# Performance work log

Hardware: AMD Instinct MI355X
Metric: run time of the kernel (lower is better)

Reference implementation:

```python
import jax, jax.numpy as jnp
import numpy as np

S, B, D, N, DH = 2048, 2, 1024, 16, 64  # seq, batch, d_model, n_head, d_head
LN_EPS = 1e-5


def setup_inputs() -> dict:
    key = jax.random.key(0)
    ks = jax.random.split(key, 8)
    h = jax.random.normal(ks[0], (S, B, D), dtype=jnp.float32)
    Wq = jax.random.normal(ks[1], (D, N * DH), dtype=jnp.float32) * 0.02
    Wkv = jax.random.normal(ks[2], (D, 2 * N * DH), dtype=jnp.float32) * 0.02
    Wo = jax.random.normal(ks[3], (N * DH, D), dtype=jnp.float32) * 0.02
    ln_gamma = jnp.ones((D,), dtype=jnp.float32)
    ln_beta = jnp.zeros((D,), dtype=jnp.float32)
    # persistent compressive-memory state from a previous segment
    memory = jax.random.normal(ks[4], (B, N, DH, DH), dtype=jnp.float32)
    # normalization is a sum of (elu(k)+1) over ~S positions -> strictly positive, O(S)
    mem_norm = jax.random.uniform(ks[5], (B, 1, N, DH), dtype=jnp.float32) * S + 1.0
    gate_beta = jnp.ones((1,), dtype=jnp.float32) * 0.01  # beta_eps
    return {"h": h, "Wq": Wq, "Wkv": Wkv, "Wo": Wo, "ln_gamma": ln_gamma,
            "ln_beta": ln_beta, "memory": memory, "mem_norm": mem_norm,
            "gate_beta": gate_beta}


def reference(h, Wq, Wkv, Wo, ln_gamma, ln_beta, memory, mem_norm, gate_beta):
    scale = 1.0 / np.sqrt(DH).astype(np.float32)
    # projections (pre_lnorm=False, mems=None -> c == h)
    q = (h @ Wq).reshape(S, B, N, DH)
    k, v = jnp.split(h @ Wkv, 2, axis=-1)
    k = k.reshape(S, B, N, DH)
    v = v.reshape(S, B, N, DH)
    # local quadratic attention
    score = jnp.einsum('ibnd,jbnd->ijbn', q, k) * scale  # [S,S,B,N]
    prob = jax.nn.softmax(score, axis=1)
    attn_vec = jnp.einsum('ijbn,jbnd->ibnd', prob, v).reshape(S, B, N * DH)
    # memory retrieval (NOTE: source swaps K/V in the _update_memory call;
    # it is done under no_grad -> stop_gradient here)
    cached_Q = jax.nn.elu(q.swapaxes(0, 1)) + 1.0          # [B,S,N,DH]
    num = jnp.einsum('bsnk,bnkv->bsnv', cached_Q, memory)   # [B,S,N,DH]
    den = jnp.einsum('bsnk,bvnk->bsnv', cached_Q, mem_norm)  # [B,S,N,1]
    content_A = jax.lax.stop_gradient(num / den)            # [B,S,N,DH]
    # gated injection
    g = jax.nn.sigmoid(gate_beta)                           # [1]
    inj = g * content_A.swapaxes(0, 1).reshape(S, B, N * DH) + (1.0 - g) * attn_vec
    attn_out = inj @ Wo
    # post layernorm residual
    y = h + attn_out
    mu = jnp.mean(y, axis=-1, keepdims=True)
    var = jnp.mean((y - mu) ** 2, axis=-1, keepdims=True)
    return (y - mu) / jnp.sqrt(var + LN_EPS) * ln_gamma + ln_beta
```

## Files before the change

kernel.cpp:

```cpp
#include <hip/hip_runtime.h>


typedef unsigned short ushort_t;
typedef unsigned int uint32;

typedef __bf16 bf16x8 __attribute__((ext_vector_type(8)));
typedef float f32x4 __attribute__((ext_vector_type(4)));
typedef float f32x16 __attribute__((ext_vector_type(16)));
typedef unsigned short u16x8 __attribute__((ext_vector_type(8)));
typedef unsigned short u16x4 __attribute__((ext_vector_type(4)));
typedef unsigned int u32x4 __attribute__((ext_vector_type(4)));

typedef const __attribute__((address_space(1))) void gvoid_t;
typedef __attribute__((address_space(3))) void lvoid_t;

#define S_LEN 2048
#define BATCH 2
#define NHEAD 16

__device__ __forceinline__ ushort_t f2bf(float x) {
  union { float f; unsigned u; } c; c.f = x;
  unsigned r = (c.u + 0x7FFFu + ((c.u >> 16) & 1u)) >> 16;
  return (ushort_t)r;
}
__device__ __forceinline__ float bf2f(ushort_t v) {
  union { unsigned u; float f; } c; c.u = ((unsigned)v) << 16;
  return c.f;
}

__global__ __launch_bounds__(256) void k_cvt_h(const float* __restrict__ src,
                                               ushort_t* __restrict__ dst, int n4) {
  int idx = blockIdx.x * 256 + threadIdx.x;
  if (idx >= n4) return;
  float4 v = ((const float4*)src)[idx];
  u16x4 o; o[0] = f2bf(v.x); o[1] = f2bf(v.y); o[2] = f2bf(v.z); o[3] = f2bf(v.w);
  ((u16x4*)dst)[idx] = o;
}

__global__ __launch_bounds__(256) void k_cvt_wT3(const float* __restrict__ Wq,
                                                 const float* __restrict__ Wkv,
                                                 const float* __restrict__ Wo,
                                                 ushort_t* __restrict__ wT,
                                                 ushort_t* __restrict__ woT) {
  const int z = blockIdx.z;
  const float* W;
  ushort_t* WT;
  int N;
  if (z == 0)      { W = Wq;  WT = wT;                          N = 1024; }
  else if (z == 1) { W = Wkv; WT = wT + (size_t)1024 * 1024;    N = 2048; }
  else             { W = Wo;  WT = woT;                         N = 1024; }
  const int K = 1024;
  if (blockIdx.x * 32 >= N) return;
  __shared__ float tile[32][33];
  const int n0 = blockIdx.x * 32, k0 = blockIdx.y * 32;
  const int tx = threadIdx.x & 31, ty = threadIdx.x >> 5;
#pragma unroll
  for (int r = 0; r < 32; r += 8)
    tile[ty + r][tx] = W[(size_t)(k0 + ty + r) * N + n0 + tx];
  __syncthreads();
#pragma unroll
  for (int r = 0; r < 32; r += 8)
    WT[(size_t)(n0 + ty + r) * K + k0 + tx] = f2bf(tile[tx][ty + r]);
}

template <int OUT_BF16>
__global__ __launch_bounds__(256) void k_gemm_bt(const ushort_t* __restrict__ A,
                                                 const ushort_t* __restrict__ B,
                                                 void* __restrict__ Cv, int M, int N, int K,
                                                 int nbx) {
  __shared__ __attribute__((aligned(16))) ushort_t As[128 * 32];
  __shared__ __attribute__((aligned(16))) ushort_t Bs[128 * 32];
  const int per = gridDim.x >> 3;
  const int fl = (blockIdx.x & 7) * per + (blockIdx.x >> 3);
  const int m0 = (fl / nbx) * 128, n0 = (fl % nbx) * 128;
  const int tid = threadIdx.x, w = tid >> 6, lane = tid & 63;
  const int wm = (w >> 1) * 64, wn = (w & 1) * 64;
  const int l15 = lane & 15, l4 = lane >> 4;
  f32x4 acc[4][4];
#pragma unroll
  for (int i = 0; i < 4; ++i)
#pragma unroll
    for (int j = 0; j < 4; ++j)
#pragma unroll
      for (int r = 0; r < 4; ++r) acc[i][j][r] = 0.f;

  for (int k0 = 0; k0 < K; k0 += 32) {
    __syncthreads();
#pragma unroll
    for (int r = 0; r < 2; ++r) {
      int c = r * 256 + w * 64 + lane;
      const ushort_t* ga = A + (size_t)(m0 + (c >> 2)) * K + k0 + (c & 3) * 8;
      const ushort_t* gb = B + (size_t)(n0 + (c >> 2)) * K + k0 + (c & 3) * 8;
      __builtin_amdgcn_global_load_lds((gvoid_t*)ga, (lvoid_t*)(As + (r * 256 + w * 64) * 8), 16, 0, 0);
      __builtin_amdgcn_global_load_lds((gvoid_t*)gb, (lvoid_t*)(Bs + (r * 256 + w * 64) * 8), 16, 0, 0);
    }
    __syncthreads();
    bf16x8 af[4], bfr[4];
#pragma unroll
    for (int i = 0; i < 4; ++i) af[i] = *(const bf16x8*)&As[(wm + i * 16 + l15) * 32 + l4 * 8];
#pragma unroll
    for (int j = 0; j < 4; ++j) bfr[j] = *(const bf16x8*)&Bs[(wn + j * 16 + l15) * 32 + l4 * 8];
#pragma unroll
    for (int i = 0; i < 4; ++i)
#pragma unroll
      for (int j = 0; j < 4; ++j)
        acc[i][j] = __builtin_amdgcn_mfma_f32_16x16x32_bf16(af[i], bfr[j], acc[i][j], 0, 0, 0);
  }
#pragma unroll
  for (int i = 0; i < 4; ++i)
#pragma unroll
    for (int j = 0; j < 4; ++j)
#pragma unroll
      for (int r = 0; r < 4; ++r) {
        int row = m0 + wm + i * 16 + l4 * 4 + r;
        int col = n0 + wn + j * 16 + l15;
        if (OUT_BF16)
          ((ushort_t*)Cv)[(size_t)row * N + col] = f2bf(acc[i][j][r]);
        else
          ((float*)Cv)[(size_t)row * N + col] = acc[i][j][r];
      }
}

__global__ __launch_bounds__(256) void k_gemm64(const ushort_t* __restrict__ A,
                                                const ushort_t* __restrict__ B,
                                                float* __restrict__ C, int M, int N, int K,
                                                int nbx) {
  __shared__ __attribute__((aligned(16))) ushort_t As[64 * 32];
  __shared__ __attribute__((aligned(16))) ushort_t Bs[128 * 32];
  const int per = gridDim.x >> 3;
  const int fl = (blockIdx.x & 7) * per + (blockIdx.x >> 3);
  const int m0 = (fl / nbx) * 64, n0 = (fl % nbx) * 128;
  const int tid = threadIdx.x, w = tid >> 6, lane = tid & 63;
  const int wn = w * 32;
  const int l15 = lane & 15, l4 = lane >> 4;
  f32x4 acc[4][2];
#pragma unroll
  for (int i = 0; i < 4; ++i)
#pragma unroll
    for (int j = 0; j < 2; ++j)
#pragma unroll
      for (int r = 0; r < 4; ++r) acc[i][j][r] = 0.f;

  for (int k0 = 0; k0 < K; k0 += 32) {
    __syncthreads();
    {
      int c = w * 64 + lane;
      const ushort_t* ga = A + (size_t)(m0 + (c >> 2)) * K + k0 + (c & 3) * 8;
      __builtin_amdgcn_global_load_lds((gvoid_t*)ga, (lvoid_t*)(As + w * 512), 16, 0, 0);
#pragma unroll
      for (int r = 0; r < 2; ++r) {
        int c2 = r * 256 + w * 64 + lane;
        const ushort_t* gb = B + (size_t)(n0 + (c2 >> 2)) * K + k0 + (c2 & 3) * 8;
        __builtin_amdgcn_global_load_lds((gvoid_t*)gb, (lvoid_t*)(Bs + r * 2048 + w * 512), 16, 0, 0);
      }
    }
    __syncthreads();
    bf16x8 af[4], bfr[2];
#pragma unroll
    for (int i = 0; i < 4; ++i) af[i] = *(const bf16x8*)&As[(i * 16 + l15) * 32 + l4 * 8];
#pragma unroll
    for (int j = 0; j < 2; ++j) bfr[j] = *(const bf16x8*)&Bs[(wn + j * 16 + l15) * 32 + l4 * 8];
#pragma unroll
    for (int i = 0; i < 4; ++i)
#pragma unroll
      for (int j = 0; j < 2; ++j)
        acc[i][j] = __builtin_amdgcn_mfma_f32_16x16x32_bf16(af[i], bfr[j], acc[i][j], 0, 0, 0);
  }
#pragma unroll
  for (int i = 0; i < 4; ++i)
#pragma unroll
    for (int j = 0; j < 2; ++j)
#pragma unroll
      for (int r = 0; r < 4; ++r)
        C[(size_t)(m0 + i * 16 + l4 * 4 + r) * N + n0 + wn + j * 16 + l15] = acc[i][j][r];
}

__global__ __launch_bounds__(256) void k_vt(const ushort_t* __restrict__ qkv,
                                            ushort_t* __restrict__ vt) {
  __shared__ uint32 tile[64 * 65];
  const int jt = blockIdx.x, bn = blockIdx.y, b = bn & 1, n = bn >> 1;
  const int tid = threadIdx.x;
  const int j0 = jt * 64;
#pragma unroll
  for (int rr = 0; rr < 2; ++rr) {
    int lin = rr * 2048 + tid * 8;
    int j = lin >> 6, d0 = lin & 63;
    u16x8 v = *(const u16x8*)(qkv + (size_t)(j0 + j) * 6144 + b * 3072 + 2048 + n * 64 + d0);
#pragma unroll
    for (int e = 0; e < 8; ++e) tile[j * 65 + d0 + e] = v[e];
  }
  __syncthreads();
#pragma unroll
  for (int rr = 0; rr < 2; ++rr) {
    int lin = rr * 2048 + tid * 8;
    int d = lin >> 6, jj = lin & 63;
    u16x8 o;
#pragma unroll
    for (int e = 0; e < 8; ++e) o[e] = (ushort_t)tile[(jj + e) * 65 + d];
    *(u16x8*)(vt + ((size_t)bn * 64 + d) * 2048 + j0 + jj) = o;
  }
}

__device__ __forceinline__ void stage_k(const ushort_t* __restrict__ qkv, ushort_t* kw,
                                        int j0, int b, int n, int w, int lane) {
#pragma unroll
  for (int r = 0; r < 2; ++r) {
    int jb_ = w * 16 + r * 8;
    int jb8 = w * 2 + r;
    const ushort_t* ksrc = qkv + (size_t)(j0 + jb_ + (lane >> 3)) * 6144 + b * 3072 + n * 64 + 1024
                           + ((((lane & 7) ^ (lane >> 3) ^ jb8) & 7) << 3);
    __builtin_amdgcn_global_load_lds((gvoid_t*)ksrc, (lvoid_t*)(kw + jb_ * 64), 16, 0, 0);
  }
}
__device__ __forceinline__ void stage_vt(const ushort_t* __restrict__ vt, ushort_t* vw,
                                         int j0, int bn, int w, int lane) {
#pragma unroll
  for (int r = 0; r < 2; ++r) {
    int db_ = w * 16 + r * 8;
    int jb8 = w * 2 + r;
    const ushort_t* vsrc = vt + ((size_t)bn * 64 + db_ + (lane >> 3)) * 2048 + j0
                           + ((((lane & 7) ^ (lane >> 3) ^ jb8) & 7) << 3);
    __builtin_amdgcn_global_load_lds((gvoid_t*)vsrc, (lvoid_t*)(vw + db_ * 64), 16, 0, 0);
  }
}

__global__ __launch_bounds__(256, 4) void k_attn(const ushort_t* __restrict__ qkv,
                                                 const ushort_t* __restrict__ vt,
                                                 ushort_t* o0, ushort_t* o1,
                                                 float* __restrict__ l0,
                                                 float* __restrict__ l1) {
  __shared__ __attribute__((aligned(16))) ushort_t Ks[2][4096];
  __shared__ __attribute__((aligned(16))) ushort_t VTs[2][4096];
  const int bn = blockIdx.y, b = bn & 1, n = bn >> 1, z = blockIdx.z;
  const int tid = threadIdx.x, w = tid >> 6, lane = tid & 63;
  const int l31 = lane & 31, h = lane >> 5;
  const int qrow = blockIdx.x * 128 + w * 32 + l31;
  const size_t qoff = (size_t)qrow * 6144 + b * 3072 + n * 64;
  const float CEXP = 0.18033688011113723f;
  bf16x8 qf[4];
#pragma unroll
  for (int ks = 0; ks < 4; ++ks) {
    u16x8 qv = *(const u16x8*)(qkv + qoff + ks * 16 + h * 8);
    union { u16x8 u; bf16x8 v; } cu;
#pragma unroll
    for (int e = 0; e < 8; ++e) cu.u[e] = f2bf(bf2f(qv[e]) * CEXP);
    qf[ks] = cu.v;
  }
  const int fA = (l31 & 7) ^ (l31 >> 3);
  const int fB = fA ^ 4;

  const int t0 = z * 16;
  stage_k(qkv, Ks[0], t0 * 64, b, n, w, lane);
  stage_vt(vt, VTs[0], t0 * 64, bn, w, lane);
  __syncthreads();

  f32x16 oacc[2];
#pragma unroll
  for (int r = 0; r < 16; ++r) { oacc[0][r] = 0.f; oacc[1][r] = 0.f; }
  float lsum = 0.f;

  for (int t = 0; t < 16; ++t) {
    const ushort_t* Kb = Ks[t & 1];
    const ushort_t* Vb = VTs[t & 1];
    if (t < 15) {
      stage_k(qkv, Ks[(t + 1) & 1], (t0 + t + 1) * 64, b, n, w, lane);
      stage_vt(vt, VTs[(t + 1) & 1], (t0 + t + 1) * 64, bn, w, lane);
    }
#pragma unroll
    for (int jb = 0; jb < 2; ++jb) {
      f32x16 sv;
#pragma unroll
      for (int r = 0; r < 16; ++r) sv[r] = 0.f;
      const int rb = (jb * 32 + l31) * 64;
      const int fj = jb ? fB : fA;
      __builtin_amdgcn_s_setprio(1);
#pragma unroll
      for (int ks = 0; ks < 4; ++ks) {
        bf16x8 kf = *(const bf16x8*)&Kb[rb + ((((ks << 1) | h) ^ fj) << 3)];
        sv = __builtin_amdgcn_mfma_f32_32x32x16_bf16(kf, qf[ks], sv, 0, 0, 0);
      }
      __builtin_amdgcn_s_setprio(0);
#pragma unroll
      for (int r = 0; r < 16; ++r) sv[r] = __builtin_amdgcn_exp2f(sv[r]);
#pragma unroll
      for (int ks2 = 0; ks2 < 2; ++ks2) {
        const int q0 = ks2 * 2;
        uint32 X0, X1, Y0, Y1;
        asm volatile("v_cvt_pk_bf16_f32 %0, %1, %2" : "=v"(X0) : "v"(sv[q0 * 4 + 0]), "v"(sv[q0 * 4 + 1]));
        asm volatile("v_cvt_pk_bf16_f32 %0, %1, %2" : "=v"(X1) : "v"(sv[q0 * 4 + 2]), "v"(sv[q0 * 4 + 3]));
        asm volatile("v_cvt_pk_bf16_f32 %0, %1, %2" : "=v"(Y0) : "v"(sv[(q0 + 1) * 4 + 0]), "v"(sv[(q0 + 1) * 4 + 1]));
        asm volatile("v_cvt_pk_bf16_f32 %0, %1, %2" : "=v"(Y1) : "v"(sv[(q0 + 1) * 4 + 2]), "v"(sv[(q0 + 1) * 4 + 3]));
        asm volatile("v_permlane32_swap_b32 %0, %1" : "+v"(X0), "+v"(Y0));
        asm volatile("v_permlane32_swap_b32 %0, %1" : "+v"(X1), "+v"(Y1));
        union { u32x4 u; bf16x8 v; } pf;
        pf.u[0] = X0; pf.u[1] = X1; pf.u[2] = Y0; pf.u[3] = Y1;
        const int c = ((jb * 2 + ks2) << 1) | h;
        bf16x8 vf0 = *(const bf16x8*)&Vb[l31 * 64 + ((c ^ fA) << 3)];
        bf16x8 vf1 = *(const bf16x8*)&Vb[(32 + l31) * 64 + ((c ^ fB) << 3)];
        __builtin_amdgcn_s_setprio(1);
        oacc[0] = __builtin_amdgcn_mfma_f32_32x32x16_bf16(vf0, pf.v, oacc[0], 0, 0, 0);
        oacc[1] = __builtin_amdgcn_mfma_f32_32x32x16_bf16(vf1, pf.v, oacc[1], 0, 0, 0);
        __builtin_amdgcn_s_setprio(0);
      }
      float ls[8];
#pragma unroll
      for (int r = 0; r < 8; ++r) ls[r] = sv[r] + sv[r + 8];
#pragma unroll
      for (int st = 4; st >= 1; st >>= 1)
#pragma unroll
        for (int r = 0; r < st; ++r) ls[r] += ls[r + st];
      lsum += ls[0];
    }
    if (t < 15) __syncthreads();
  }
  const float l_run = lsum + __shfl_xor(lsum, 32);

  ushort_t* op = (z == 0) ? (o0 + (size_t)qrow * 2048 + b * 1024 + n * 64)
                          : (o1 + (size_t)qrow * 6144 + b * 3072 + 2048 + n * 64);
#pragma unroll
  for (int db = 0; db < 2; ++db)
#pragma unroll
    for (int qq = 0; qq < 4; ++qq) {
      u16x4 st;
#pragma unroll
      for (int m = 0; m < 4; ++m) st[m] = f2bf(oacc[db][qq * 4 + m]);
      *(u16x4*)(op + db * 32 + qq * 8 + h * 4) = st;
    }
  if (h == 0) {
    float* lp = (z == 0) ? l0 : l1;
    lp[qrow * 32 + bn] = l_run;
  }
}

__global__ __launch_bounds__(256) void k_gate2(const ushort_t* __restrict__ qkv,
                                               const ushort_t* __restrict__ o0,
                                               const float* __restrict__ l0,
                                               const float* __restrict__ l1,
                                               const float* __restrict__ mem,
                                               const float* __restrict__ mnorm,
                                               const float* __restrict__ gbeta,
                                               ushort_t* __restrict__ inj) {
  const int bn = blockIdx.y, b = bn & 1, n = bn >> 1;
  const int tid = threadIdx.x, w = tid >> 6, lane = tid & 63;
  const int l31 = lane & 31, h = lane >> 5;
  const int qrow = blockIdx.x * 128 + w * 32 + l31;
  const size_t qoff = (size_t)qrow * 6144 + b * 3072 + n * 64;

  float den = 0.f;
  bf16x8 cqf[4];
  const float* nrm = mnorm + (size_t)(b * NHEAD + n) * 64;
#pragma unroll
  for (int ks = 0; ks < 4; ++ks) {
    u16x8 qv = *(const u16x8*)(qkv + qoff + ks * 16 + h * 8);
    union { u16x8 u; bf16x8 v; } cu;
#pragma unroll
    for (int e = 0; e < 8; ++e) {
      float x = bf2f(qv[e]);
      float c = (x > 0.f) ? (x + 1.f) : __builtin_amdgcn_exp2f(x * 1.4426950408889634f);
      cu.u[e] = f2bf(c);
      den += c * nrm[ks * 16 + h * 8 + e];
    }
    cqf[ks] = cu.v;
  }
  den += __shfl_xor(den, 32);

  const float* mb = mem + (size_t)(b * NHEAD + n) * 4096;
  f32x16 accv[2];
#pragma unroll
  for (int r = 0; r < 16; ++r) { accv[0][r] = 0.f; accv[1][r] = 0.f; }
#pragma unroll
  for (int db = 0; db < 2; ++db)
#pragma unroll
    for (int ks = 0; ks < 4; ++ks) {
      union { u16x8 u; bf16x8 v; } af;
#pragma unroll
      for (int e = 0; e < 8; ++e)
        af.u[e] = f2bf(mb[(size_t)(ks * 16 + h * 8 + e) * 64 + db * 32 + l31]);
      accv[db] = __builtin_amdgcn_mfma_f32_32x32x16_bf16(af.v, cqf[ks], accv[db], 0, 0, 0);
    }

  const float lsum = l0[qrow * 32 + bn] + l1[qrow * 32 + bn];
  float g = 1.f / (1.f + expf(-gbeta[0]));
  float rden = 1.f / den, invl = 1.f / lsum;
  const ushort_t* p0 = o0 + (size_t)qrow * 2048 + b * 1024 + n * 64;
  const ushort_t* p1 = qkv + (size_t)qrow * 6144 + b * 3072 + 2048 + n * 64;
  ushort_t* op = inj + (size_t)qrow * 2048 + b * 1024 + n * 64;
#pragma unroll
  for (int db = 0; db < 2; ++db)
#pragma unroll
    for (int qq = 0; qq < 4; ++qq) {
      const int off = db * 32 + qq * 8 + h * 4;
      u16x4 a0 = *(const u16x4*)(p0 + off);
      u16x4 a1 = *(const u16x4*)(p1 + off);
      u16x4 st;
#pragma unroll
      for (int m = 0; m < 4; ++m) {
        float av = (bf2f(a0[m]) + bf2f(a1[m])) * invl;
        float content = accv[db][qq * 4 + m] * rden;
        st[m] = f2bf(g * content + (1.f - g) * av);
      }
      *(u16x4*)(op + off) = st;
    }
}

__global__ __launch_bounds__(256) void k_ln(const float* __restrict__ h,
                                            const float* __restrict__ ao,
                                            const float* __restrict__ gam,
                                            const float* __restrict__ bet,
                                            float* __restrict__ out) {
  const int m = blockIdx.x, t = threadIdx.x;
  const int lane = t & 63, w = t >> 6;
  __shared__ float redS[4], redQ[4];
  const size_t base = (size_t)m * 1024;
  float4 hv = ((const float4*)(h + base))[t];
  float4 avv = ((const float4*)(ao + base))[t];
  float y0 = hv.x + avv.x, y1 = hv.y + avv.y, y2 = hv.z + avv.z, y3 = hv.w + avv.w;
  float s = y0 + y1 + y2 + y3;
  float sq = y0 * y0 + y1 * y1 + y2 * y2 + y3 * y3;
#pragma unroll
  for (int mk = 32; mk >= 1; mk >>= 1) { s += __shfl_xor(s, mk); sq += __shfl_xor(sq, mk); }
  if (lane == 0) { redS[w] = s; redQ[w] = sq; }
  __syncthreads();
  float Ssum = redS[0] + redS[1] + redS[2] + redS[3];
  float Qsum = redQ[0] + redQ[1] + redQ[2] + redQ[3];
  float mu = Ssum * (1.f / 1024.f);
  float var = Qsum * (1.f / 1024.f) - mu * mu;
  float rstd = rsqrtf(var + 1e-5f);
  float4 g = ((const float4*)gam)[t];
  float4 bt = ((const float4*)bet)[t];
  float4 o;
  o.x = (y0 - mu) * rstd * g.x + bt.x;
  o.y = (y1 - mu) * rstd * g.y + bt.y;
  o.z = (y2 - mu) * rstd * g.z + bt.z;
  o.w = (y3 - mu) * rstd * g.w + bt.w;
  ((float4*)(out + base))[t] = o;
}

extern "C" void kernel_launch(void* const* d_in, const int* in_sizes, int n_in,
                              void* d_out, int out_size, void* d_ws, size_t ws_size,
                              hipStream_t stream) {
  const float* h = (const float*)d_in[0];
  const float* Wq = (const float*)d_in[1];
  const float* Wkv = (const float*)d_in[2];
  const float* Wo = (const float*)d_in[3];
  const float* gam = (const float*)d_in[4];
  const float* bet = (const float*)d_in[5];
  const float* mem = (const float*)d_in[6];
  const float* mnorm = (const float*)d_in[7];
  const float* gbeta = (const float*)d_in[8];
  float* out = (float*)d_out;

  char* ws = (char*)d_ws;
  ushort_t* hb  = (ushort_t*)(ws);
  ushort_t* wT  = (ushort_t*)(ws + (size_t)(8u << 20));
  ushort_t* woT = (ushort_t*)(ws + (size_t)(14u << 20));
  ushort_t* qkv = (ushort_t*)(ws + (size_t)(16u << 20));
  float*    ao  = (float*)   (ws + (size_t)(16u << 20));
  ushort_t* vtb = (ushort_t*)(ws + (size_t)(40u << 20));
  ushort_t* o0  = hb;
  float*    l0  = (float*)(ws + (size_t)(8u << 20));
  float*    l1  = (float*)(ws + (size_t)(8u << 20) + (1u << 18));
  ushort_t* inj = vtb;

  k_cvt_h<<<4096, 256, 0, stream>>>(h, hb, 1048576);
  k_cvt_wT3<<<dim3(64, 32, 3), 256, 0, stream>>>(Wq, Wkv, Wo, wT, woT);
  k_gemm_bt<1><<<768, 256, 0, stream>>>(hb, wT, (void*)qkv, 4096, 3072, 1024, 24);
  k_vt<<<dim3(32, 32), 256, 0, stream>>>(qkv, vtb);
  k_attn<<<dim3(16, 32, 2), 256, 0, stream>>>(qkv, vtb, o0, qkv, l0, l1);
  k_gate2<<<dim3(16, 32), 256, 0, stream>>>(qkv, o0, l0, l1, mem, mnorm, gbeta, inj);
  k_gemm64<<<512, 256, 0, stream>>>(inj, woT, ao, 4096, 1024, 1024, 8);
  k_ln<<<4096, 256, 0, stream>>>(h, ao, gam, bet, out);
}
```

Measured before the change: 150.4 us.

## Deepen GEMM K-tile to 64 with XOR-swizzled LDS and hoist attention load pointers

```diff
diff --git a/kernel.cpp b/kernel.cpp
--- a/kernel.cpp
+++ b/kernel.cpp
@@ -68,14 +68,15 @@
                                                  const ushort_t* __restrict__ B,
                                                  void* __restrict__ Cv, int M, int N, int K,
                                                  int nbx) {
-  __shared__ __attribute__((aligned(16))) ushort_t As[128 * 32];
-  __shared__ __attribute__((aligned(16))) ushort_t Bs[128 * 32];
+  __shared__ __attribute__((aligned(16))) ushort_t As[128 * 64];
+  __shared__ __attribute__((aligned(16))) ushort_t Bs[128 * 64];
   const int per = gridDim.x >> 3;
   const int fl = (blockIdx.x & 7) * per + (blockIdx.x >> 3);
   const int m0 = (fl / nbx) * 128, n0 = (fl % nbx) * 128;
   const int tid = threadIdx.x, w = tid >> 6, lane = tid & 63;
   const int wm = (w >> 1) * 64, wn = (w & 1) * 64;
   const int l15 = lane & 15, l4 = lane >> 4;
+  const int sw = ((lane & 7) ^ (lane >> 3)) << 3;
   f32x4 acc[4][4];
 #pragma unroll
   for (int i = 0; i < 4; ++i)
@@ -84,27 +85,36 @@
 #pragma unroll
       for (int r = 0; r < 4; ++r) acc[i][j][r] = 0.f;
 
-  for (int k0 = 0; k0 < K; k0 += 32) {
+  for (int k0 = 0; k0 < K; k0 += 64) {
     __syncthreads();
 #pragma unroll
-    for (int r = 0; r < 2; ++r) {
-      int c = r * 256 + w * 64 + lane;
-      const ushort_t* ga = A + (size_t)(m0 + (c >> 2)) * K + k0 + (c & 3) * 8;
-      const ushort_t* gb = B + (size_t)(n0 + (c >> 2)) * K + k0 + (c & 3) * 8;
-      __builtin_amdgcn_global_load_lds((gvoid_t*)ga, (lvoid_t*)(As + (r * 256 + w * 64) * 8), 16, 0, 0);
-      __builtin_amdgcn_global_load_lds((gvoid_t*)gb, (lvoid_t*)(Bs + (r * 256 + w * 64) * 8), 16, 0, 0);
+    for (int r = 0; r < 4; ++r) {
+      int rowb = r * 32 + w * 8;
+      const ushort_t* ga = A + (size_t)(m0 + rowb + (lane >> 3)) * K + k0 + sw;
+      const ushort_t* gb = B + (size_t)(n0 + rowb + (lane >> 3)) * K + k0 + sw;
+      __builtin_amdgcn_global_load_lds((gvoid_t*)ga, (lvoid_t*)(As + rowb * 64), 16, 0, 0);
+      __builtin_amdgcn_global_load_lds((gvoid_t*)gb, (lvoid_t*)(Bs + rowb * 64), 16, 0, 0);
     }
     __syncthreads();
-    bf16x8 af[4], bfr[4];
-#pragma unroll
-    for (int i = 0; i < 4; ++i) af[i] = *(const bf16x8*)&As[(wm + i * 16 + l15) * 32 + l4 * 8];
-#pragma unroll
-    for (int j = 0; j < 4; ++j) bfr[j] = *(const bf16x8*)&Bs[(wn + j * 16 + l15) * 32 + l4 * 8];
-#pragma unroll
-    for (int i = 0; i < 4; ++i)
-#pragma unroll
-      for (int j = 0; j < 4; ++j)
-        acc[i][j] = __builtin_amdgcn_mfma_f32_16x16x32_bf16(af[i], bfr[j], acc[i][j], 0, 0, 0);
+#pragma unroll
+    for (int kk = 0; kk < 2; ++kk) {
+      bf16x8 af[4], bfr[4];
+#pragma unroll
+      for (int i = 0; i < 4; ++i) {
+        int row = wm + i * 16 + l15;
+        af[i] = *(const bf16x8*)&As[row * 64 + (((kk * 4 + l4) ^ (row & 7)) << 3)];
+      }
+#pragma unroll
+      for (int j = 0; j < 4; ++j) {
+        int row = wn + j * 16 + l15;
+        bfr[j] = *(const bf16x8*)&Bs[row * 64 + (((kk * 4 + l4) ^ (row & 7)) << 3)];
+      }
+#pragma unroll
+      for (int i = 0; i < 4; ++i)
+#pragma unroll
+        for (int j = 0; j < 4; ++j)
+          acc[i][j] = __builtin_amdgcn_mfma_f32_16x16x32_bf16(af[i], bfr[j], acc[i][j], 0, 0, 0);
+    }
   }
 #pragma unroll
   for (int i = 0; i < 4; ++i)
@@ -198,29 +208,6 @@
 #pragma unroll
     for (int e = 0; e < 8; ++e) o[e] = (ushort_t)tile[(jj + e) * 65 + d];
     *(u16x8*)(vt + ((size_t)bn * 64 + d) * 2048 + j0 + jj) = o;
-  }
-}
-
-__device__ __forceinline__ void stage_k(const ushort_t* __restrict__ qkv, ushort_t* kw,
-                                        int j0, int b, int n, int w, int lane) {
-#pragma unroll
-  for (int r = 0; r < 2; ++r) {
-    int jb_ = w * 16 + r * 8;
-    int jb8 = w * 2 + r;
-    const ushort_t* ksrc = qkv + (size_t)(j0 + jb_ + (lane >> 3)) * 6144 + b * 3072 + n * 64 + 1024
-                           + ((((lane & 7) ^ (lane >> 3) ^ jb8) & 7) << 3);
-    __builtin_amdgcn_global_load_lds((gvoid_t*)ksrc, (lvoid_t*)(kw + jb_ * 64), 16, 0, 0);
-  }
-}
-__device__ __forceinline__ void stage_vt(const ushort_t* __restrict__ vt, ushort_t* vw,
-                                         int j0, int bn, int w, int lane) {
-#pragma unroll
-  for (int r = 0; r < 2; ++r) {
-    int db_ = w * 16 + r * 8;
-    int jb8 = w * 2 + r;
-    const ushort_t* vsrc = vt + ((size_t)bn * 64 + db_ + (lane >> 3)) * 2048 + j0
-                           + ((((lane & 7) ^ (lane >> 3) ^ jb8) & 7) << 3);
-    __builtin_amdgcn_global_load_lds((gvoid_t*)vsrc, (lvoid_t*)(vw + db_ * 64), 16, 0, 0);
   }
 }
 
@@ -250,8 +237,19 @@
   const int fB = fA ^ 4;
 
   const int t0 = z * 16;
-  stage_k(qkv, Ks[0], t0 * 64, b, n, w, lane);
-  stage_vt(vt, VTs[0], t0 * 64, bn, w, lane);
+  const int sw0 = (((lane & 7) ^ (lane >> 3) ^ (w * 2)) & 7) << 3;
+  const int sw1 = (((lane & 7) ^ (lane >> 3) ^ (w * 2 + 1)) & 7) << 3;
+  const ushort_t* kp0 = qkv + (size_t)(t0 * 64 + w * 16 + (lane >> 3)) * 6144 + b * 3072 + n * 64 + 1024 + sw0;
+  const ushort_t* kp1 = qkv + (size_t)(t0 * 64 + w * 16 + 8 + (lane >> 3)) * 6144 + b * 3072 + n * 64 + 1024 + sw1;
+  const ushort_t* vp0 = vt + ((size_t)bn * 64 + w * 16 + (lane >> 3)) * 2048 + t0 * 64 + sw0;
+  const ushort_t* vp1 = vt + ((size_t)bn * 64 + w * 16 + 8 + (lane >> 3)) * 2048 + t0 * 64 + sw1;
+  const size_t KSTRIDE = (size_t)64 * 6144;
+
+  __builtin_amdgcn_global_load_lds((gvoid_t*)kp0, (lvoid_t*)(Ks[0] + (w * 16) * 64), 16, 0, 0);
+  __builtin_amdgcn_global_load_lds((gvoid_t*)kp1, (lvoid_t*)(Ks[0] + (w * 16 + 8) * 64), 16, 0, 0);
+  __builtin_amdgcn_global_load_lds((gvoid_t*)vp0, (lvoid_t*)(VTs[0] + (w * 16) * 64), 16, 0, 0);
+  __builtin_amdgcn_global_load_lds((gvoid_t*)vp1, (lvoid_t*)(VTs[0] + (w * 16 + 8) * 64), 16, 0, 0);
+  kp0 += KSTRIDE; kp1 += KSTRIDE; vp0 += 64; vp1 += 64;
   __syncthreads();
 
   f32x16 oacc[2];
@@ -263,8 +261,13 @@
     const ushort_t* Kb = Ks[t & 1];
     const ushort_t* Vb = VTs[t & 1];
     if (t < 15) {
-      stage_k(qkv, Ks[(t + 1) & 1], (t0 + t + 1) * 64, b, n, w, lane);
-      stage_vt(vt, VTs[(t + 1) & 1], (t0 + t + 1) * 64, bn, w, lane);
+      ushort_t* kw = Ks[(t + 1) & 1];
+      ushort_t* vw = VTs[(t + 1) & 1];
+      __builtin_amdgcn_global_load_lds((gvoid_t*)kp0, (lvoid_t*)(kw + (w * 16) * 64), 16, 0, 0);
+      __builtin_amdgcn_global_load_lds((gvoid_t*)kp1, (lvoid_t*)(kw + (w * 16 + 8) * 64), 16, 0, 0);
+      __builtin_amdgcn_global_load_lds((gvoid_t*)vp0, (lvoid_t*)(vw + (w * 16) * 64), 16, 0, 0);
+      __builtin_amdgcn_global_load_lds((gvoid_t*)vp1, (lvoid_t*)(vw + (w * 16 + 8) * 64), 16, 0, 0);
+      kp0 += KSTRIDE; kp1 += KSTRIDE; vp0 += 64; vp1 += 64;
     }
 #pragma unroll
     for (int jb = 0; jb < 2; ++jb) {
```

New measurement: 144.4 us. 4.0% less time.
